# Kernel optimization log

Hardware: AMD Instinct MI355X
Metric: run time of the kernel (lower is better)

The kernel has to match this reference:

```python
import jax, jax.numpy as jnp
import numpy as np

DIM = 24
HID = 256
N = 4096
NUM_LO = DIM * (DIM - 1) // 2  # 276
NEG = -0.01  # slope used in the hand-written Jacobians (source uses -0.01, NOT the fwd leaky slope 0.01; faithful)


def _linear_params(key, out_dim, in_dim):
    kw, kb = jax.random.split(key)
    s = 1.0 / np.sqrt(in_dim)
    W = jax.random.uniform(kw, (out_dim, in_dim), jnp.float32, -s, s)
    b = jax.random.uniform(kb, (out_dim,), jnp.float32, -s, s)
    return W, b


def setup_inputs() -> dict:
    key = jax.random.key(0)
    k = jax.random.split(key, 7)
    W1, b1 = _linear_params(k[0], HID, DIM)
    W2, b2 = _linear_params(k[1], HID, HID)
    WG, bG = _linear_params(k[2], DIM, HID)
    WLd, bLd = _linear_params(k[3], DIM, HID)
    WLo, bLo = _linear_params(k[4], NUM_LO, HID)
    q = jax.random.normal(k[5], (N, DIM), jnp.float32)
    q_dot = jax.random.normal(k[6], (N, DIM), jnp.float32)
    return {"q": q, "q_dot": q_dot, "W1": W1, "b1": b1, "W2": W2, "b2": b2,
            "WG": WG, "bG": bG, "WLd": WLd, "bLd": bLd, "WLo": WLo, "bLo": bLo}


def _forward(q, q_dot, W1, b1, W2, b2, WG, bG, WLd, bLd, WLo, bLo):
    n, d = q.shape
    tr, tc = np.tril_indices(d, -1)  # row-major strict-lower order == torch mask-flatten order
    di = np.arange(d)
    # MLP trunk (torch leaky_relu default slope 0.01)
    h1 = jax.nn.leaky_relu(q @ W1.T + b1)                       # [n,HID]
    h2 = jax.nn.leaky_relu(h1 @ W2.T + b2)                      # [n,HID]
    h3 = h2 @ WLd.T + bLd                                       # [n,d]
    g = h2 @ WG.T + bG                                          # [n,d]
    Ld = jax.nn.softplus(h3)                                    # [n,d]
    Lo = h2 @ WLo.T + bLo                                       # [n,NUM_LO]
    # Lower-triangular L (diag_embed(Ld) + masked strict-lower fill)
    L = jnp.zeros((n, d, d), q.dtype).at[:, tr, tc].set(Lo).at[:, di, di].set(Ld)
    # Hand-written Jacobian chain; diag_embed(v)@W == v[:,:,None]*W (direct elementwise scaling)
    dR1 = jnp.where(h1 > 0, 1.0, NEG)
    J1 = dR1[:, :, None] * W1                                    # dh1/dq  [n,HID,d]
    dR2 = jnp.where(h2 > 0, 1.0, NEG)
    J2 = dR2[:, :, None] * jnp.einsum('ij,njd->nid', W2, J1)     # dh2/dq  [n,HID,d]
    sig = jax.nn.sigmoid(h3)
    dld_dq = sig[:, :, None] * jnp.einsum('ij,njd->nid', WLd, J2)  # [n,d,d]
    dlo_dq = jnp.einsum('oj,njd->nod', WLo, J2)                  # [n,NUM_LO,d]
    dld_dt = jnp.einsum('nid,nd->ni', dld_dq, q_dot)             # [n,d]
    dlo_dt = jnp.einsum('nod,nd->no', dlo_dq, q_dot)             # [n,NUM_LO]
    dL_dt = jnp.zeros((n, d, d), q.dtype).at[:, tr, tc].set(dlo_dt).at[:, di, di].set(dld_dt)
    # 4D assembly: torch does L[L==1] = dlo_dq.view(-1), which reinterprets the (lo, q_idx)
    # flat buffer in (q_idx, tril_pos) order -> plain reshape replicates that exactly.
    vals = dlo_dq.reshape(n, d, NUM_LO)
    dld_dq_p = dld_dq.transpose(0, 2, 1)                         # [n, d_q, d_ld]
    dL_dq = jnp.zeros((n, d, d, d), q.dtype).at[:, :, tr, tc].set(vals).at[:, :, di, di].set(dld_dq_p)
    eye = jnp.eye(d, dtype=q.dtype)
    M = L @ L.transpose(0, 2, 1) + 1e-9 * eye
    dM_dt = L @ dL_dt.transpose(0, 2, 1) + dL_dt @ L.transpose(0, 2, 1)
    # Quadratic term. torch: q_dot.repeat(d,1)/L.repeat(d,1,1) index as (i % n) while
    # dL_dq.view(n*d,d,d) indexes as (i // d, i % d) -> replicate exactly (faithful).
    idx = jnp.arange(n * d) % n
    qd_r = q_dot[idx]                                            # [n*d, d]
    L_r = L[idx]                                                 # [n*d, d, d]
    dL_i = dL_dq.reshape(n * d, d, d)
    S = dL_i @ L_r.transpose(0, 2, 1) + L_r @ dL_i.transpose(0, 2, 1)
    quad = jnp.einsum('bi,bij,bj->b', qd_r, S, qd_r).reshape(n, d)
    c = jnp.einsum('nij,nj->ni', dM_dt, q_dot) - 0.5 * quad
    return M, c, g


def reference(q, q_dot, W1, b1, W2, b2, WG, bG, WLd, bLd, WLo, bLo):
    return _forward(q, q_dot, W1, b1, W2, b2, WG, bG, WLd, bLd, WLo, bLo)
```

## Files before the change

kernel.cpp:

```cpp
#include <hip/hip_runtime.h>
#include <math.h>

#define DIM 24
#define HID 256
#define NLO 276
#define NSAMP 4096
#define C_OFF 2359296
#define G_OFF 2457600

#define OFF_W2T  0
#define OFF_WHT  65536
#define OFF_W1T  149504
#define OFF_W2FH 155648
#define OFF_W2FL 188416
#define OFF_WEFH 221184
#define OFF_WEFL 262144
#define OFF_REC  303104
#define REC_STRIDE 640

typedef __attribute__((ext_vector_type(8))) short bf16x8;
typedef __attribute__((ext_vector_type(4))) float f32x4;

__device__ __forceinline__ float leaky(float x){ return x > 0.f ? x : 0.01f*x; }
__device__ __forceinline__ unsigned short f2b(float f){
  unsigned u = __float_as_uint(f);
  return (unsigned short)((u + 0x7FFFu + ((u >> 16) & 1u)) >> 16);
}
__device__ __forceinline__ float b2f(unsigned short h){ return __uint_as_float(((unsigned)h) << 16); }

__global__ __launch_bounds__(256) void k0_prep(
    const float* __restrict__ W1, const float* __restrict__ W2,
    const float* __restrict__ WG, const float* __restrict__ WLd,
    const float* __restrict__ WLo, float* __restrict__ ws)
{
  const int tid = blockIdx.x*256 + threadIdx.x;
  const int nth = gridDim.x*256;
  for (int f = tid; f < 65536; f += nth){ int k = f>>8, i = f&255; ws[OFF_W2T+f] = W2[i*256+k]; }
  for (int f = tid; f < 83968; f += nth){
    int k = f/328, c = f%328; float v = 0.f;
    if (c < 24) v = WLd[c*256+k];
    else if (c < 48) v = WG[(c-24)*256+k];
    else if (c < 324) v = WLo[(c-48)*256+k];
    ws[OFF_WHT+f] = v;
  }
  for (int f = tid; f < 6144; f += nth){ int d = f>>8, i = f&255; ws[OFF_W1T+f] = W1[i*24+d]; }
  unsigned short* W2FH = (unsigned short*)(ws + OFF_W2FH);
  unsigned short* W2FL = (unsigned short*)(ws + OFF_W2FL);
  for (int e = tid; e < 65536; e += nth){
    int j = e&7, l = (e>>3)&63, kb = (e>>9)&7, mt = e>>12;
    int m = mt*16 + (l&15), k = kb*32 + ((l>>4)&3)*8 + j;
    float v = W2[m*256 + k];
    unsigned short h = f2b(v);
    W2FH[e] = h; W2FL[e] = f2b(v - b2f(h));
  }
  unsigned short* WEFH = (unsigned short*)(ws + OFF_WEFH);
  unsigned short* WEFL = (unsigned short*)(ws + OFF_WEFL);
  for (int e = tid; e < 81920; e += nth){
    int j = e&7, l = (e>>3)&63, kb = (e>>9)&7, mt = e>>12;
    int r = mt*16 + (l&15), k = kb*32 + ((l>>4)&3)*8 + j;
    float v = 0.f;
    if (r < 24) v = WLd[r*256+k]; else if (r < 300) v = WLo[(r-24)*256+k];
    unsigned short h = f2b(v);
    WEFH[e] = h; WEFL[e] = f2b(v - b2f(h));
  }
}

__global__ __launch_bounds__(256) void k1_fwd(
    const float* __restrict__ q, const float* __restrict__ qd,
    const float* __restrict__ b1, const float* __restrict__ b2,
    const float* __restrict__ bG, const float* __restrict__ bLd,
    const float* __restrict__ bLo, float* __restrict__ ws,
    float* __restrict__ out)
{
  const int n = blockIdx.x, t = threadIdx.x;
  const int w = t >> 6, l = t & 63;
  const float* W2T = ws + OFF_W2T;
  const float* WHT = ws + OFF_WHT;
  const float* W1T = ws + OFF_W1T;
  float* rec = ws + OFF_REC + (size_t)n*REC_STRIDE;

  __shared__ float q_s[DIM], qd_s[DIM], h1_s[HID], h2_s[HID], h3_s[DIM], lo_s[NLO], L_s[DIM*DIM];
  if (t < DIM){ q_s[t] = q[n*DIM+t]; qd_s[t] = qd[n*DIM+t]; }
  __syncthreads();
  {
    float s = b1[t];
    #pragma unroll
    for (int d = 0; d < DIM; ++d) s += W1T[d*256 + t]*q_s[d];
    unsigned long long b = __ballot(s > 0.f);
    if (l == 0){ ((unsigned*)rec)[2*w] = (unsigned)b; ((unsigned*)rec)[2*w+1] = (unsigned)(b >> 32); }
    h1_s[t] = leaky(s);
  }
  __syncthreads();
  {
    float s = b2[t];
    const float4* h = (const float4*)h1_s;
    for (int k4 = 0; k4 < HID/4; ++k4){
      float4 hv = h[k4];
      int k = 4*k4;
      s += W2T[(k+0)*256+t]*hv.x + W2T[(k+1)*256+t]*hv.y
         + W2T[(k+2)*256+t]*hv.z + W2T[(k+3)*256+t]*hv.w;
    }
    unsigned long long b = __ballot(s > 0.f);
    if (l == 0){ ((unsigned*)rec)[8+2*w] = (unsigned)b; ((unsigned*)rec)[8+2*w+1] = (unsigned)(b >> 32); }
    h2_s[t] = leaky(s);
  }
  __syncthreads();
  for (int c = t; c < 324; c += 256){
    float acc = 0.f;
    const float4* h = (const float4*)h2_s;
    for (int k4 = 0; k4 < HID/4; ++k4){
      float4 hv = h[k4];
      int k = 4*k4;
      acc += WHT[(k+0)*328+c]*hv.x + WHT[(k+1)*328+c]*hv.y
           + WHT[(k+2)*328+c]*hv.z + WHT[(k+3)*328+c]*hv.w;
    }
    if (c < 24){
      acc += bLd[c];
      h3_s[c] = acc;
      rec[16 + c] = 1.f/(1.f + expf(-acc));
    } else if (c < 48){
      out[G_OFF + n*DIM + (c-24)] = acc + bG[c-24];
    } else {
      lo_s[c-48] = acc + bLo[c-48];
    }
  }
  __syncthreads();
  for (int idx = t; idx < DIM*DIM; idx += 256){
    int r = idx/DIM, c = idx%DIM; float v = 0.f;
    if (r == c){ float x = h3_s[r]; v = fmaxf(x, 0.f) + log1pf(expf(-fabsf(x))); }
    else if (r > c) v = lo_s[r*(r-1)/2 + c];
    L_s[idx] = v; rec[64 + idx] = v;
  }
  __syncthreads();
  for (int idx = t; idx < DIM*DIM; idx += 256){
    int r = idx/DIM, c = idx%DIM, km = min(r, c);
    float acc = (r == c) ? 1e-9f : 0.f;
    for (int k = 0; k <= km; ++k) acc += L_s[r*DIM+k]*L_s[c*DIM+k];
    out[n*DIM*DIM + idx] = acc;
  }
  if (t < DIM){
    float acc = 0.f;
    for (int r = t; r < DIM; ++r) acc += qd_s[r]*L_s[r*DIM+t];
    rec[40 + t] = acc;
  }
}

__global__ __launch_bounds__(256, 2) void k2_jac(
    const float* __restrict__ q_dot, const float* __restrict__ W1g,
    float* __restrict__ ws, float* __restrict__ out)
{
  const int n0 = blockIdx.x*2, t = threadIdx.x;
  const int w = t >> 6, l = t & 63;
  const int l15 = l & 15, l4g = (l >> 4) & 3;
  const float* REC = ws + OFF_REC;

  __shared__ __align__(16) char pool[59808];
  __shared__ float dld2[2][576];
  __shared__ float qd2[2][24], u2[2][24], sig2[2][24], dld_dt2[2][24], w12[2][24];
  __shared__ unsigned msk[2][16];
  unsigned short* BH = (unsigned short*)pool;
  unsigned short* BL = (unsigned short*)(pool + 25344);
  float* dlo2   = (float*)pool;
  float* dLdt2  = (float*)(pool + 52992);
  float* dlo_dt2= (float*)(pool + 57600);

  if (t < 32) msk[t>>4][t&15] = ((const unsigned*)(REC + (size_t)(n0 + (t>>4))*REC_STRIDE))[t&15];
  if (t < 48){
    int s = t/24, i = t%24;
    const float* rc = REC + (size_t)(n0+s)*REC_STRIDE;
    sig2[s][i] = rc[16+i]; u2[s][i] = rc[40+i]; qd2[s][i] = q_dot[(n0+s)*24+i];
  }
  __syncthreads();

  {
    float w1r[24];
    #pragma unroll
    for (int d = 0; d < 24; ++d) w1r[d] = W1g[t*24 + d];
    float dr0 = ((msk[0][t>>5] >> (t&31)) & 1u) ? 1.f : -0.01f;
    float dr1 = ((msk[1][t>>5] >> (t&31)) & 1u) ? 1.f : -0.01f;
    #pragma unroll
    for (int c = 0; c < 48; ++c){
      int s = c >= 24, d = c - 24*s;
      float f = (s ? dr1 : dr0) * w1r[d];
      unsigned short h = f2b(f);
      BH[c*264 + t] = h;
      BL[c*264 + t] = f2b(f - b2f(h));
    }
  }
  __syncthreads();

  f32x4 accD[4][3];
  #pragma unroll
  for (int i = 0; i < 4; ++i)
    #pragma unroll
    for (int nt = 0; nt < 3; ++nt) accD[i][nt] = (f32x4){0.f,0.f,0.f,0.f};
  {
    const bf16x8* AHp = (const bf16x8*)(ws + OFF_W2FH);
    const bf16x8* ALp = (const bf16x8*)(ws + OFF_W2FL);
    for (int kb = 0; kb < 8; ++kb){
      bf16x8 AH[4], AL[4], BHf[3], BLf[3];
      #pragma unroll
      for (int i = 0; i < 4; ++i){
        int mt = 4*w + i;
        AH[i] = AHp[(mt*8+kb)*64 + l];
        AL[i] = ALp[(mt*8+kb)*64 + l];
      }
      #pragma unroll
      for (int nt = 0; nt < 3; ++nt){
        int off = (nt*16 + l15)*264 + kb*32 + l4g*8;
        BHf[nt] = *(const bf16x8*)(BH + off);
        BLf[nt] = *(const bf16x8*)(BL + off);
      }
      #pragma unroll
      for (int i = 0; i < 4; ++i)
        #pragma unroll
        for (int nt = 0; nt < 3; ++nt){
          accD[i][nt] = __builtin_amdgcn_mfma_f32_16x16x32_bf16(AH[i], BHf[nt], accD[i][nt], 0, 0, 0);
          accD[i][nt] = __builtin_amdgcn_mfma_f32_16x16x32_bf16(AH[i], BLf[nt], accD[i][nt], 0, 0, 0);
          accD[i][nt] = __builtin_amdgcn_mfma_f32_16x16x32_bf16(AL[i], BHf[nt], accD[i][nt], 0, 0, 0);
        }
    }
  }
  __syncthreads();

  {
    unsigned short* JH = BH; unsigned short* JL = BL;
    #pragma unroll
    for (int i = 0; i < 4; ++i){
      int mt = 4*w + i;
      int m0 = mt*16 + 4*l4g;
      int bb = m0 & 31;
      #pragma unroll
      for (int nt = 0; nt < 3; ++nt){
        int c = nt*16 + l15;
        int s = c >= 24;
        unsigned word = msk[s][8 + (mt>>1)];
        unsigned short hs[4], ls[4];
        #pragma unroll
        for (int r = 0; r < 4; ++r){
          float sc = ((word >> (bb + r)) & 1u) ? 1.f : -0.01f;
          float v = sc * accD[i][nt][r];
          hs[r] = f2b(v); ls[r] = f2b(v - b2f(hs[r]));
        }
        *(uint2*)(JH + c*264 + m0) = make_uint2((unsigned)hs[0] | ((unsigned)hs[1]<<16),
                                                (unsigned)hs[2] | ((unsigned)hs[3]<<16));
        *(uint2*)(JL + c*264 + m0) = make_uint2((unsigned)ls[0] | ((unsigned)ls[1]<<16),
                                                (unsigned)ls[2] | ((unsigned)ls[3]<<16));
      }
    }
  }
  __syncthreads();

  f32x4 accE[5][3];
  #pragma unroll
  for (int i = 0; i < 5; ++i)
    #pragma unroll
    for (int nt = 0; nt < 3; ++nt) accE[i][nt] = (f32x4){0.f,0.f,0.f,0.f};
  {
    const bf16x8* AHp = (const bf16x8*)(ws + OFF_WEFH);
    const bf16x8* ALp = (const bf16x8*)(ws + OFF_WEFL);
    for (int kb = 0; kb < 8; ++kb){
      bf16x8 AH[5], AL[5], BHf[3], BLf[3];
      #pragma unroll
      for (int i = 0; i < 5; ++i){
        int mt = 5*w + i;
        AH[i] = AHp[(mt*8+kb)*64 + l];
        AL[i] = ALp[(mt*8+kb)*64 + l];
      }
      #pragma unroll
      for (int nt = 0; nt < 3; ++nt){
        int off = (nt*16 + l15)*264 + kb*32 + l4g*8;
        BHf[nt] = *(const bf16x8*)(BH + off);
        BLf[nt] = *(const bf16x8*)(BL + off);
      }
      #pragma unroll
      for (int i = 0; i < 5; ++i)
        #pragma unroll
        for (int nt = 0; nt < 3; ++nt){
          accE[i][nt] = __builtin_amdgcn_mfma_f32_16x16x32_bf16(AH[i], BHf[nt], accE[i][nt], 0, 0, 0);
          accE[i][nt] = __builtin_amdgcn_mfma_f32_16x16x32_bf16(AH[i], BLf[nt], accE[i][nt], 0, 0, 0);
          accE[i][nt] = __builtin_amdgcn_mfma_f32_16x16x32_bf16(AL[i], BHf[nt], accE[i][nt], 0, 0, 0);
        }
    }
  }
  __syncthreads();

  #pragma unroll
  for (int i = 0; i < 5; ++i){
    int mt = 5*w + i;
    #pragma unroll
    for (int nt = 0; nt < 3; ++nt){
      int c = nt*16 + l15;
      int s = c >= 24, d = c - 24*s;
      #pragma unroll
      for (int r = 0; r < 4; ++r){
        int re = mt*16 + 4*l4g + r;
        float v = accE[i][nt][r];
        if (re < 24) dld2[s][re*24 + d] = sig2[s][re]*v;
        else if (re < 300) dlo2[s*6624 + (re-24)*24 + d] = v;
      }
    }
  }
  __syncthreads();

  for (int o2 = t; o2 < 2*NLO; o2 += 256){
    int s = o2 / NLO, o = o2 % NLO;
    float a = 0.f;
    #pragma unroll
    for (int d = 0; d < 24; ++d) a += dlo2[s*6624 + o*24 + d]*qd2[s][d];
    dlo_dt2[s*NLO + o] = a;
  }
  if (t < 48){
    int s = t/24, i = t%24;
    float a = 0.f;
    #pragma unroll
    for (int d = 0; d < 24; ++d) a += dld2[s][i*24+d]*qd2[s][d];
    dld_dt2[s][i] = a;
  }
  __syncthreads();
  for (int idx = t; idx < 1152; idx += 256){
    int s = idx/576, e = idx%576, r = e/24, cc = e%24;
    float v = 0.f;
    if (r == cc) v = dld_dt2[s][r]; else if (r > cc) v = dlo_dt2[s*NLO + r*(r-1)/2 + cc];
    dLdt2[s*576 + e] = v;
  }
  __syncthreads();
  if (t < 48){
    int s = t/24, i = t%24;
    float a = 0.f;
    #pragma unroll
    for (int j = 0; j < 24; ++j) a += qd2[s][j]*dLdt2[s*576 + j*24 + i];
    w12[s][i] = a;
  }
  __syncthreads();
  if (t < 48){
    int s = t/24, i = t%24;
    int n = n0 + s;
    const float* Lrow = REC + (size_t)n*REC_STRIDE + 64 + i*24;
    float cs = 0.f;
    #pragma unroll
    for (int k = 0; k < 24; ++k) cs += Lrow[k]*w12[s][k] + dLdt2[s*576 + i*24 + k]*u2[s][k];
    const int m = (n*24 + i) & (NSAMP-1);
    const float* um  = REC + (size_t)m*REC_STRIDE + 40;
    const float* qdm = q_dot + m*24;
    const float* vb  = dlo2 + s*6624 + i*NLO;
    float quad = 0.f;
    for (int c2 = 0; c2 < 24; ++c2){
      float v = qdm[c2]*dld2[s][c2*24 + i];
      for (int r = c2+1; r < 24; ++r) v += qdm[r]*vb[r*(r-1)/2 + c2];
      quad += um[c2]*v;
    }
    out[C_OFF + n*24 + i] = cs - quad;
  }
}

extern "C" void kernel_launch(void* const* d_in, const int* in_sizes, int n_in,
                              void* d_out, int out_size, void* d_ws, size_t ws_size,
                              hipStream_t stream)
{
  const float* q   = (const float*)d_in[0];
  const float* qd  = (const float*)d_in[1];
  const float* W1  = (const float*)d_in[2];
  const float* b1  = (const float*)d_in[3];
  const float* W2  = (const float*)d_in[4];
  const float* b2  = (const float*)d_in[5];
  const float* WG  = (const float*)d_in[6];
  const float* bG  = (const float*)d_in[7];
  const float* WLd = (const float*)d_in[8];
  const float* bLd = (const float*)d_in[9];
  const float* WLo = (const float*)d_in[10];
  const float* bLo = (const float*)d_in[11];
  float* out = (float*)d_out;
  float* ws  = (float*)d_ws;

  k0_prep<<<256, 256, 0, stream>>>(W1, W2, WG, WLd, WLo, ws);
  k1_fwd<<<NSAMP, 256, 0, stream>>>(q, qd, b1, b2, bG, bLd, bLo, ws, out);
  k2_jac<<<NSAMP/2, 256, 0, stream>>>(qd, W1, ws, out);
}
```

Measured before the change: 290.4 us.

## Batch forward MLP over 32 samples with split-fp16 MFMA and compact records

The forward kernel used one block per sample doing scalar fp32 GEMVs. It now processes 32 samples per block as MFMA GEMMs, using an fp16 hi/lo split with a scaled residual to keep near-fp32 accuracy. The per-sample record is compacted to store packed strict-lower L values, and the M = L L^T computation moves into the Jacobian kernel. The Jacobian kernel also pads its shared buffers to a stride of 25, works directly on packed triangular data without materialising dL/dt, and splits the quadratic term across 4 thread groups. The trade-offs are extra MFMA passes for the hi/lo split, some fp16 range and precision risk, and more work placed in the second kernel.

New measurement: 290.7 us. No clear change (+0.1%).

```diff
diff --git a/kernel.cpp b/kernel.cpp
--- a/kernel.cpp
+++ b/kernel.cpp
@@ -8,17 +8,21 @@
 #define C_OFF 2359296
 #define G_OFF 2457600
 
-#define OFF_W2T  0
-#define OFF_WHT  65536
-#define OFF_W1T  149504
-#define OFF_W2FH 155648
-#define OFF_W2FL 188416
-#define OFF_WEFH 221184
-#define OFF_WEFL 262144
-#define OFF_REC  303104
-#define REC_STRIDE 640
+#define OFF_W2FH 0
+#define OFF_W2FL 32768
+#define OFF_WEFH 65536
+#define OFF_WEFL 106496
+#define OFF_W1H16 147456
+#define OFF_W1L16 151552
+#define OFF_W2H16 155648
+#define OFF_W2L16 188416
+#define OFF_WHH16 221184
+#define OFF_WHL16 264192
+#define OFF_REC  307200
+#define REC_STRIDE 364
 
 typedef __attribute__((ext_vector_type(8))) short bf16x8;
+typedef __attribute__((ext_vector_type(8))) _Float16 f16x8;
 typedef __attribute__((ext_vector_type(4))) float f32x4;
 
 __device__ __forceinline__ float leaky(float x){ return x > 0.f ? x : 0.01f*x; }
@@ -27,6 +31,11 @@
   return (unsigned short)((u + 0x7FFFu + ((u >> 16) & 1u)) >> 16);
 }
 __device__ __forceinline__ float b2f(unsigned short h){ return __uint_as_float(((unsigned)h) << 16); }
+__device__ __forceinline__ void f2h2(float v, unsigned short* hi, unsigned short* lo){
+  _Float16 h = (_Float16)v;
+  _Float16 l = (_Float16)((v - (float)h) * 4096.f);
+  *hi = *(unsigned short*)&h; *lo = *(unsigned short*)&l;
+}
 
 __global__ __launch_bounds__(256) void k0_prep(
     const float* __restrict__ W1, const float* __restrict__ W2,
@@ -35,113 +44,255 @@
 {
   const int tid = blockIdx.x*256 + threadIdx.x;
   const int nth = gridDim.x*256;
-  for (int f = tid; f < 65536; f += nth){ int k = f>>8, i = f&255; ws[OFF_W2T+f] = W2[i*256+k]; }
-  for (int f = tid; f < 83968; f += nth){
-    int k = f/328, c = f%328; float v = 0.f;
-    if (c < 24) v = WLd[c*256+k];
-    else if (c < 48) v = WG[(c-24)*256+k];
-    else if (c < 324) v = WLo[(c-48)*256+k];
-    ws[OFF_WHT+f] = v;
-  }
-  for (int f = tid; f < 6144; f += nth){ int d = f>>8, i = f&255; ws[OFF_W1T+f] = W1[i*24+d]; }
   unsigned short* W2FH = (unsigned short*)(ws + OFF_W2FH);
   unsigned short* W2FL = (unsigned short*)(ws + OFF_W2FL);
   for (int e = tid; e < 65536; e += nth){
-    int j = e&7, l = (e>>3)&63, kb = (e>>9)&7, mt = e>>12;
-    int m = mt*16 + (l&15), k = kb*32 + ((l>>4)&3)*8 + j;
-    float v = W2[m*256 + k];
+    int j=e&7, l=(e>>3)&63, kb=(e>>9)&7, mt=e>>12;
+    int m = mt*16+(l&15), k = kb*32+((l>>4)&3)*8+j;
+    float v = W2[m*256+k];
     unsigned short h = f2b(v);
-    W2FH[e] = h; W2FL[e] = f2b(v - b2f(h));
+    W2FH[e]=h; W2FL[e]=f2b(v-b2f(h));
   }
   unsigned short* WEFH = (unsigned short*)(ws + OFF_WEFH);
   unsigned short* WEFL = (unsigned short*)(ws + OFF_WEFL);
   for (int e = tid; e < 81920; e += nth){
-    int j = e&7, l = (e>>3)&63, kb = (e>>9)&7, mt = e>>12;
-    int r = mt*16 + (l&15), k = kb*32 + ((l>>4)&3)*8 + j;
+    int j=e&7, l=(e>>3)&63, kb=(e>>9)&7, mt=e>>12;
+    int r = mt*16+(l&15), k = kb*32+((l>>4)&3)*8+j;
     float v = 0.f;
     if (r < 24) v = WLd[r*256+k]; else if (r < 300) v = WLo[(r-24)*256+k];
     unsigned short h = f2b(v);
-    WEFH[e] = h; WEFL[e] = f2b(v - b2f(h));
+    WEFH[e]=h; WEFL[e]=f2b(v-b2f(h));
+  }
+  unsigned short* W1H = (unsigned short*)(ws + OFF_W1H16);
+  unsigned short* W1L = (unsigned short*)(ws + OFF_W1L16);
+  for (int e = tid; e < 8192; e += nth){
+    int j=e&7, l=(e>>3)&63, mt=e>>9;
+    int m = mt*16+(l&15), k = ((l>>4)&3)*8+j;
+    float v = (k < 24) ? W1[m*24+k] : 0.f;
+    f2h2(v, &W1H[e], &W1L[e]);
+  }
+  unsigned short* W2H = (unsigned short*)(ws + OFF_W2H16);
+  unsigned short* W2L = (unsigned short*)(ws + OFF_W2L16);
+  for (int e = tid; e < 65536; e += nth){
+    int j=e&7, l=(e>>3)&63, kb=(e>>9)&7, mt=e>>12;
+    int m = mt*16+(l&15), k = kb*32+((l>>4)&3)*8+j;
+    f2h2(W2[m*256+k], &W2H[e], &W2L[e]);
+  }
+  unsigned short* WHH = (unsigned short*)(ws + OFF_WHH16);
+  unsigned short* WHL = (unsigned short*)(ws + OFF_WHL16);
+  for (int e = tid; e < 86016; e += nth){
+    int j=e&7, l=(e>>3)&63, kb=(e>>9)&7, mt=e>>12;
+    int rr = mt*16+(l&15), k = kb*32+((l>>4)&3)*8+j;
+    float v = 0.f;
+    if (rr < 24) v = WLd[rr*256+k];
+    else if (rr < 48) v = WG[(rr-24)*256+k];
+    else if (rr < 324) v = WLo[(rr-48)*256+k];
+    f2h2(v, &WHH[e], &WHL[e]);
   }
 }
 
 __global__ __launch_bounds__(256) void k1_fwd(
-    const float* __restrict__ q, const float* __restrict__ qd,
+    const float* __restrict__ q, const float* __restrict__ qd_g,
     const float* __restrict__ b1, const float* __restrict__ b2,
     const float* __restrict__ bG, const float* __restrict__ bLd,
     const float* __restrict__ bLo, float* __restrict__ ws,
     float* __restrict__ out)
 {
-  const int n = blockIdx.x, t = threadIdx.x;
-  const int w = t >> 6, l = t & 63;
-  const float* W2T = ws + OFF_W2T;
-  const float* WHT = ws + OFF_WHT;
-  const float* W1T = ws + OFF_W1T;
-  float* rec = ws + OFF_REC + (size_t)n*REC_STRIDE;
-
-  __shared__ float q_s[DIM], qd_s[DIM], h1_s[HID], h2_s[HID], h3_s[DIM], lo_s[NLO], L_s[DIM*DIM];
-  if (t < DIM){ q_s[t] = q[n*DIM+t]; qd_s[t] = qd[n*DIM+t]; }
-  __syncthreads();
-  {
-    float s = b1[t];
-    #pragma unroll
-    for (int d = 0; d < DIM; ++d) s += W1T[d*256 + t]*q_s[d];
-    unsigned long long b = __ballot(s > 0.f);
-    if (l == 0){ ((unsigned*)rec)[2*w] = (unsigned)b; ((unsigned*)rec)[2*w+1] = (unsigned)(b >> 32); }
-    h1_s[t] = leaky(s);
-  }
-  __syncthreads();
-  {
-    float s = b2[t];
-    const float4* h = (const float4*)h1_s;
-    for (int k4 = 0; k4 < HID/4; ++k4){
-      float4 hv = h[k4];
-      int k = 4*k4;
-      s += W2T[(k+0)*256+t]*hv.x + W2T[(k+1)*256+t]*hv.y
-         + W2T[(k+2)*256+t]*hv.z + W2T[(k+3)*256+t]*hv.w;
-    }
-    unsigned long long b = __ballot(s > 0.f);
-    if (l == 0){ ((unsigned*)rec)[8+2*w] = (unsigned)b; ((unsigned*)rec)[8+2*w+1] = (unsigned)(b >> 32); }
-    h2_s[t] = leaky(s);
-  }
-  __syncthreads();
-  for (int c = t; c < 324; c += 256){
-    float acc = 0.f;
-    const float4* h = (const float4*)h2_s;
-    for (int k4 = 0; k4 < HID/4; ++k4){
-      float4 hv = h[k4];
-      int k = 4*k4;
-      acc += WHT[(k+0)*328+c]*hv.x + WHT[(k+1)*328+c]*hv.y
-           + WHT[(k+2)*328+c]*hv.z + WHT[(k+3)*328+c]*hv.w;
-    }
-    if (c < 24){
-      acc += bLd[c];
-      h3_s[c] = acc;
-      rec[16 + c] = 1.f/(1.f + expf(-acc));
-    } else if (c < 48){
-      out[G_OFF + n*DIM + (c-24)] = acc + bG[c-24];
-    } else {
-      lo_s[c-48] = acc + bLo[c-48];
-    }
-  }
-  __syncthreads();
-  for (int idx = t; idx < DIM*DIM; idx += 256){
-    int r = idx/DIM, c = idx%DIM; float v = 0.f;
-    if (r == c){ float x = h3_s[r]; v = fmaxf(x, 0.f) + log1pf(expf(-fabsf(x))); }
-    else if (r > c) v = lo_s[r*(r-1)/2 + c];
-    L_s[idx] = v; rec[64 + idx] = v;
-  }
-  __syncthreads();
-  for (int idx = t; idx < DIM*DIM; idx += 256){
-    int r = idx/DIM, c = idx%DIM, km = min(r, c);
-    float acc = (r == c) ? 1e-9f : 0.f;
-    for (int k = 0; k <= km; ++k) acc += L_s[r*DIM+k]*L_s[c*DIM+k];
-    out[n*DIM*DIM + idx] = acc;
-  }
-  if (t < DIM){
-    float acc = 0.f;
-    for (int r = t; r < DIM; ++r) acc += qd_s[r]*L_s[r*DIM+t];
-    rec[40 + t] = acc;
+  const int s0 = blockIdx.x*32, t = threadIdx.x;
+  const int w = t>>6, l = t&63, l15 = l&15, l4g = (l>>4)&3;
+  float* REC = ws + OFF_REC;
+
+  __shared__ __align__(16) char pool[33792];
+  __shared__ float qd_s[32][24];
+  __shared__ float Ld_s[32][24];
+  __shared__ unsigned char mb[32][64];
+  unsigned short* BQH = (unsigned short*)pool;
+  unsigned short* BQL = BQH + 1280;
+  unsigned short* BH2 = (unsigned short*)pool;
+  unsigned short* BL2 = BH2 + 8448;
+
+  for (int f = t; f < 768; f += 256){
+    float v = q[s0*24 + f];
+    int n = f/24, k = f%24;
+    f2h2(v, &BQH[n*40+k], &BQL[n*40+k]);
+    ((float*)qd_s)[f] = qd_g[s0*24 + f];
+  }
+  { int n = t>>3, k = 24 + (t&7); BQH[n*40+k]=0; BQL[n*40+k]=0; }
+  __syncthreads();
+
+  f32x4 aH[4][2], aX[4][2];
+  #pragma unroll
+  for (int i=0;i<4;++i) for (int nt=0;nt<2;++nt){ aH[i][nt]=(f32x4){0,0,0,0}; aX[i][nt]=(f32x4){0,0,0,0}; }
+  {
+    const f16x8* WH = (const f16x8*)(ws + OFF_W1H16);
+    const f16x8* WL = (const f16x8*)(ws + OFF_W1L16);
+    f16x8 Af[4], Al[4], Bh[2], Bl[2];
+    #pragma unroll
+    for (int i=0;i<4;++i){ int mt=w+4*i; Af[i]=WH[mt*64+l]; Al[i]=WL[mt*64+l]; }
+    #pragma unroll
+    for (int nt=0;nt<2;++nt){
+      int off=(nt*16+l15)*40 + l4g*8;
+      Bh[nt]=*(const f16x8*)(BQH+off); Bl[nt]=*(const f16x8*)(BQL+off);
+    }
+    #pragma unroll
+    for (int i=0;i<4;++i)
+      #pragma unroll
+      for (int nt=0;nt<2;++nt){
+        aH[i][nt]=__builtin_amdgcn_mfma_f32_16x16x32_f16(Af[i],Bh[nt],aH[i][nt],0,0,0);
+        aX[i][nt]=__builtin_amdgcn_mfma_f32_16x16x32_f16(Af[i],Bl[nt],aX[i][nt],0,0,0);
+        aX[i][nt]=__builtin_amdgcn_mfma_f32_16x16x32_f16(Al[i],Bh[nt],aX[i][nt],0,0,0);
+      }
+  }
+  __syncthreads();
+  #pragma unroll
+  for (int i=0;i<4;++i){
+    int m0=(w+4*i)*16+4*l4g;
+    float4 bb = *(const float4*)(b1+m0);
+    #pragma unroll
+    for (int nt=0;nt<2;++nt){
+      int n = nt*16+l15;
+      unsigned nib=0; unsigned short hs[4], ls[4];
+      #pragma unroll
+      for (int r=0;r<4;++r){
+        float val = aH[i][nt][r] + aX[i][nt][r]*(1.f/4096.f) + ((const float*)&bb)[r];
+        if (val > 0.f) nib |= 1u<<r;
+        f2h2(leaky(val), &hs[r], &ls[r]);
+      }
+      mb[n][(m0>>2)] = (unsigned char)nib;
+      *(uint2*)(BH2 + n*264 + m0) = make_uint2((unsigned)hs[0]|((unsigned)hs[1]<<16),
+                                               (unsigned)hs[2]|((unsigned)hs[3]<<16));
+      *(uint2*)(BL2 + n*264 + m0) = make_uint2((unsigned)ls[0]|((unsigned)ls[1]<<16),
+                                               (unsigned)ls[2]|((unsigned)ls[3]<<16));
+    }
+  }
+  __syncthreads();
+  {
+    int n = t>>3, w8 = t&7; unsigned word = 0;
+    #pragma unroll
+    for (int b=0;b<8;++b) word |= (unsigned)(mb[n][w8*8+b] & 0xFu) << (4*b);
+    ((unsigned*)(REC + (size_t)(s0+n)*REC_STRIDE))[w8] = word;
+  }
+
+  #pragma unroll
+  for (int i=0;i<4;++i) for (int nt=0;nt<2;++nt){ aH[i][nt]=(f32x4){0,0,0,0}; aX[i][nt]=(f32x4){0,0,0,0}; }
+  {
+    const f16x8* WH = (const f16x8*)(ws + OFF_W2H16);
+    const f16x8* WL = (const f16x8*)(ws + OFF_W2L16);
+    for (int kb=0;kb<8;++kb){
+      f16x8 Af[4], Al[4], Bh[2], Bl[2];
+      #pragma unroll
+      for (int i=0;i<4;++i){ int mt=w+4*i; Af[i]=WH[(mt*8+kb)*64+l]; Al[i]=WL[(mt*8+kb)*64+l]; }
+      #pragma unroll
+      for (int nt=0;nt<2;++nt){
+        int off=(nt*16+l15)*264 + kb*32 + l4g*8;
+        Bh[nt]=*(const f16x8*)(BH2+off); Bl[nt]=*(const f16x8*)(BL2+off);
+      }
+      #pragma unroll
+      for (int i=0;i<4;++i)
+        #pragma unroll
+        for (int nt=0;nt<2;++nt){
+          aH[i][nt]=__builtin_amdgcn_mfma_f32_16x16x32_f16(Af[i],Bh[nt],aH[i][nt],0,0,0);
+          aX[i][nt]=__builtin_amdgcn_mfma_f32_16x16x32_f16(Af[i],Bl[nt],aX[i][nt],0,0,0);
+          aX[i][nt]=__builtin_amdgcn_mfma_f32_16x16x32_f16(Al[i],Bh[nt],aX[i][nt],0,0,0);
+        }
+    }
+  }
+  __syncthreads();
+  #pragma unroll
+  for (int i=0;i<4;++i){
+    int m0=(w+4*i)*16+4*l4g;
+    float4 bb = *(const float4*)(b2+m0);
+    #pragma unroll
+    for (int nt=0;nt<2;++nt){
+      int n = nt*16+l15;
+      unsigned nib=0; unsigned short hs[4], ls[4];
+      #pragma unroll
+      for (int r=0;r<4;++r){
+        float val = aH[i][nt][r] + aX[i][nt][r]*(1.f/4096.f) + ((const float*)&bb)[r];
+        if (val > 0.f) nib |= 1u<<r;
+        f2h2(leaky(val), &hs[r], &ls[r]);
+      }
+      mb[n][(m0>>2)] = (unsigned char)nib;
+      *(uint2*)(BH2 + n*264 + m0) = make_uint2((unsigned)hs[0]|((unsigned)hs[1]<<16),
+                                               (unsigned)hs[2]|((unsigned)hs[3]<<16));
+      *(uint2*)(BL2 + n*264 + m0) = make_uint2((unsigned)ls[0]|((unsigned)ls[1]<<16),
+                                               (unsigned)ls[2]|((unsigned)ls[3]<<16));
+    }
+  }
+  __syncthreads();
+  {
+    int n = t>>3, w8 = t&7; unsigned word = 0;
+    #pragma unroll
+    for (int b=0;b<8;++b) word |= (unsigned)(mb[n][w8*8+b] & 0xFu) << (4*b);
+    ((unsigned*)(REC + (size_t)(s0+n)*REC_STRIDE))[8+w8] = word;
+  }
+
+  for (int pass=0; pass<2; ++pass){
+    f32x4 cH[3][2], cX[3][2];
+    #pragma unroll
+    for (int i=0;i<3;++i) for (int nt=0;nt<2;++nt){ cH[i][nt]=(f32x4){0,0,0,0}; cX[i][nt]=(f32x4){0,0,0,0}; }
+    const f16x8* WH = (const f16x8*)(ws + OFF_WHH16);
+    const f16x8* WL = (const f16x8*)(ws + OFF_WHL16);
+    for (int kb=0;kb<8;++kb){
+      f16x8 Af[3], Al[3], Bh[2], Bl[2];
+      #pragma unroll
+      for (int i=0;i<3;++i){
+        int mt = w + 4*(3*pass+i);
+        if (mt < 21){ Af[i]=WH[(mt*8+kb)*64+l]; Al[i]=WL[(mt*8+kb)*64+l]; }
+      }
+      #pragma unroll
+      for (int nt=0;nt<2;++nt){
+        int off=(nt*16+l15)*264 + kb*32 + l4g*8;
+        Bh[nt]=*(const f16x8*)(BH2+off); Bl[nt]=*(const f16x8*)(BL2+off);
+      }
+      #pragma unroll
+      for (int i=0;i<3;++i){
+        int mt = w + 4*(3*pass+i);
+        if (mt < 21){
+          #pragma unroll
+          for (int nt=0;nt<2;++nt){
+            cH[i][nt]=__builtin_amdgcn_mfma_f32_16x16x32_f16(Af[i],Bh[nt],cH[i][nt],0,0,0);
+            cX[i][nt]=__builtin_amdgcn_mfma_f32_16x16x32_f16(Af[i],Bl[nt],cX[i][nt],0,0,0);
+            cX[i][nt]=__builtin_amdgcn_mfma_f32_16x16x32_f16(Al[i],Bh[nt],cX[i][nt],0,0,0);
+          }
+        }
+      }
+    }
+    #pragma unroll
+    for (int i=0;i<3;++i){
+      int mt = w + 4*(3*pass+i);
+      if (mt >= 21) continue;
+      int m0 = mt*16+4*l4g;
+      #pragma unroll
+      for (int nt=0;nt<2;++nt){
+        int n = nt*16+l15, sG = s0+n;
+        float* recn = REC + (size_t)sG*REC_STRIDE;
+        #pragma unroll
+        for (int r=0;r<4;++r){
+          int rr = m0+r;
+          float val = cH[i][nt][r] + cX[i][nt][r]*(1.f/4096.f);
+          if (rr < 24){
+            val += bLd[rr];
+            recn[16+rr] = 1.f/(1.f + expf(-val));
+            float sp = fmaxf(val,0.f) + log1pf(expf(-fabsf(val)));
+            recn[64+rr] = sp; Ld_s[n][rr] = sp;
+          } else if (rr < 48){
+            out[G_OFF + sG*24 + (rr-24)] = val + bG[rr-24];
+          } else if (rr < 324){
+            recn[88 + rr-48] = val + bLo[rr-48];
+          }
+        }
+      }
+    }
+  }
+  __syncthreads();
+
+  for (int task=t; task<768; task+=256){
+    int n = task/24, c = task%24;
+    float* recn = REC + (size_t)(s0+n)*REC_STRIDE;
+    float u = qd_s[n][c]*Ld_s[n][c];
+    for (int r=c+1; r<24; ++r) u += qd_s[n][r]*recn[88 + r*(r-1)/2 + c];
+    recn[40+c] = u;
   }
 }
 
@@ -152,23 +303,39 @@
   const int n0 = blockIdx.x*2, t = threadIdx.x;
   const int w = t >> 6, l = t & 63;
   const int l15 = l & 15, l4g = (l >> 4) & 3;
-  const float* REC = ws + OFF_REC;
-
-  __shared__ __align__(16) char pool[59808];
-  __shared__ float dld2[2][576];
+  float* REC = ws + OFF_REC;
+
+  __shared__ __align__(16) char pool[58176];
+  __shared__ float dld2v[1200];
   __shared__ float qd2[2][24], u2[2][24], sig2[2][24], dld_dt2[2][24], w12[2][24];
   __shared__ unsigned msk[2][16];
+  float* Lp = (float*)pool;
   unsigned short* BH = (unsigned short*)pool;
-  unsigned short* BL = (unsigned short*)(pool + 25344);
-  float* dlo2   = (float*)pool;
-  float* dLdt2  = (float*)(pool + 52992);
-  float* dlo_dt2= (float*)(pool + 57600);
-
-  if (t < 32) msk[t>>4][t&15] = ((const unsigned*)(REC + (size_t)(n0 + (t>>4))*REC_STRIDE))[t&15];
+  unsigned short* BL = BH + 12672;
+  float* dlo2 = (float*)pool;
+  float* dlo_dt2 = (float*)(pool + 55200);
+  float* qp = (float*)(pool + 57408);
+
+  if (t < 32) msk[t>>4][t&15] = ((const unsigned*)(REC + (size_t)(n0+(t>>4))*REC_STRIDE))[t&15];
   if (t < 48){
     int s = t/24, i = t%24;
     const float* rc = REC + (size_t)(n0+s)*REC_STRIDE;
     sig2[s][i] = rc[16+i]; u2[s][i] = rc[40+i]; qd2[s][i] = q_dot[(n0+s)*24+i];
+  }
+  for (int e = t; e < 1152; e += 256){
+    int s = e/576, rc = e%576, r = rc/24, c = rc%24;
+    const float* rr = REC + (size_t)(n0+s)*REC_STRIDE;
+    float v = 0.f;
+    if (r == c) v = rr[64+r]; else if (r > c) v = rr[88 + r*(r-1)/2 + c];
+    Lp[s*600 + r*25 + c] = v;
+  }
+  __syncthreads();
+  for (int e = t; e < 1152; e += 256){
+    int s = e/576, rc = e%576, r = rc/24, c = rc%24, km = min(r,c);
+    float acc = (r == c) ? 1e-9f : 0.f;
+    const float* Ls = Lp + s*600;
+    for (int k = 0; k <= km; ++k) acc += Ls[r*25+k]*Ls[c*25+k];
+    out[(size_t)(n0+s)*576 + rc] = acc;
   }
   __syncthreads();
 
@@ -224,7 +391,6 @@
   __syncthreads();
 
   {
-    unsigned short* JH = BH; unsigned short* JL = BL;
     #pragma unroll
     for (int i = 0; i < 4; ++i){
       int mt = 4*w + i;
@@ -242,9 +408,9 @@
           float v = sc * accD[i][nt][r];
           hs[r] = f2b(v); ls[r] = f2b(v - b2f(hs[r]));
         }
-        *(uint2*)(JH + c*264 + m0) = make_uint2((unsigned)hs[0] | ((unsigned)hs[1]<<16),
+        *(uint2*)(BH + c*264 + m0) = make_uint2((unsigned)hs[0] | ((unsigned)hs[1]<<16),
                                                 (unsigned)hs[2] | ((unsigned)hs[3]<<16));
-        *(uint2*)(JL + c*264 + m0) = make_uint2((unsigned)ls[0] | ((unsigned)ls[1]<<16),
+        *(uint2*)(BL + c*264 + m0) = make_uint2((unsigned)ls[0] | ((unsigned)ls[1]<<16),
                                                 (unsigned)ls[2] | ((unsigned)ls[3]<<16));
       }
     }
@@ -296,60 +462,64 @@
       for (int r = 0; r < 4; ++r){
         int re = mt*16 + 4*l4g + r;
         float v = accE[i][nt][r];
-        if (re < 24) dld2[s][re*24 + d] = sig2[s][re]*v;
-        else if (re < 300) dlo2[s*6624 + (re-24)*24 + d] = v;
-      }
-    }
-  }
-  __syncthreads();
-
-  for (int o2 = t; o2 < 2*NLO; o2 += 256){
-    int s = o2 / NLO, o = o2 % NLO;
+        if (re < 24) dld2v[s*600 + re*25 + d] = sig2[s][re]*v;
+        else if (re < 300) dlo2[s*6900 + (re-24)*25 + d] = v;
+      }
+    }
+  }
+  __syncthreads();
+
+  for (int o2 = t; o2 < 552; o2 += 256){
+    int s = o2/276, o = o2%276;
     float a = 0.f;
     #pragma unroll
-    for (int d = 0; d < 24; ++d) a += dlo2[s*6624 + o*24 + d]*qd2[s][d];
-    dlo_dt2[s*NLO + o] = a;
+    for (int d = 0; d < 24; ++d) a += dlo2[s*6900 + o*25 + d]*qd2[s][d];
+    dlo_dt2[s*276 + o] = a;
   }
   if (t < 48){
     int s = t/24, i = t%24;
     float a = 0.f;
     #pragma unroll
-    for (int d = 0; d < 24; ++d) a += dld2[s][i*24+d]*qd2[s][d];
+    for (int d = 0; d < 24; ++d) a += dld2v[s*600 + i*25 + d]*qd2[s][d];
     dld_dt2[s][i] = a;
   }
   __syncthreads();
-  for (int idx = t; idx < 1152; idx += 256){
-    int s = idx/576, e = idx%576, r = e/24, cc = e%24;
-    float v = 0.f;
-    if (r == cc) v = dld_dt2[s][r]; else if (r > cc) v = dlo_dt2[s*NLO + r*(r-1)/2 + cc];
-    dLdt2[s*576 + e] = v;
-  }
-  __syncthreads();
+
+  if (t < 192){
+    int g = t/48, si = t%48, s = si/24, i = si%24;
+    int n = n0 + s;
+    int m = (n*24 + i) & (NSAMP-1);
+    const float* qdm = q_dot + m*24;
+    const float* um  = REC + (size_t)m*REC_STRIDE + 40;
+    float part = 0.f;
+    for (int c2 = g; c2 < 24; c2 += 4){
+      float v = qdm[c2]*dld2v[s*600 + c2*25 + i];
+      for (int r = c2+1; r < 24; ++r){
+        int f = i*276 + r*(r-1)/2 + c2;
+        v += qdm[r]*dlo2[s*6900 + (f/24)*25 + (f%24)];
+      }
+      part += um[c2]*v;
+    }
+    qp[g*48 + si] = part;
+  }
   if (t < 48){
     int s = t/24, i = t%24;
-    float a = 0.f;
-    #pragma unroll
-    for (int j = 0; j < 24; ++j) a += qd2[s][j]*dLdt2[s*576 + j*24 + i];
+    float a = qd2[s][i]*dld_dt2[s][i];
+    for (int j = i+1; j < 24; ++j) a += qd2[s][j]*dlo_dt2[s*276 + j*(j-1)/2 + i];
     w12[s][i] = a;
   }
   __syncthreads();
+
   if (t < 48){
-    int s = t/24, i = t%24;
-    int n = n0 + s;
-    const float* Lrow = REC + (size_t)n*REC_STRIDE + 64 + i*24;
+    int s = t/24, i = t%24, n = n0 + s;
+    const float* recn = REC + (size_t)n*REC_STRIDE;
     float cs = 0.f;
-    #pragma unroll
-    for (int k = 0; k < 24; ++k) cs += Lrow[k]*w12[s][k] + dLdt2[s*576 + i*24 + k]*u2[s][k];
-    const int m = (n*24 + i) & (NSAMP-1);
-    const float* um  = REC + (size_t)m*REC_STRIDE + 40;
-    const float* qdm = q_dot + m*24;
-    const float* vb  = dlo2 + s*6624 + i*NLO;
-    float quad = 0.f;
-    for (int c2 = 0; c2 < 24; ++c2){
-      float v = qdm[c2]*dld2[s][c2*24 + i];
-      for (int r = c2+1; r < 24; ++r) v += qdm[r]*vb[r*(r-1)/2 + c2];
-      quad += um[c2]*v;
-    }
+    for (int k = 0; k < i; ++k){
+      float Lik = recn[88 + i*(i-1)/2 + k];
+      cs += Lik*w12[s][k] + dlo_dt2[s*276 + i*(i-1)/2 + k]*u2[s][k];
+    }
+    cs += recn[64+i]*w12[s][i] + dld_dt2[s][i]*u2[s][i];
+    float quad = qp[t] + qp[48+t] + qp[96+t] + qp[144+t];
     out[C_OFF + n*24 + i] = cs - quad;
   }
 }
@@ -374,6 +544,6 @@
   float* ws  = (float*)d_ws;
 
   k0_prep<<<256, 256, 0, stream>>>(W1, W2, WG, WLd, WLo, ws);
-  k1_fwd<<<NSAMP, 256, 0, stream>>>(q, qd, b1, b2, bG, bLd, bLo, ws, out);
+  k1_fwd<<<NSAMP/32, 256, 0, stream>>>(q, qd, b1, b2, bG, bLd, bLo, ws, out);
   k2_jac<<<NSAMP/2, 256, 0, stream>>>(qd, W1, ws, out);
 }
```
